# Optimization experiments

Hardware: AMD Instinct MI355X
Metric: run time of the kernel (lower is better)

## Reference

```python
import jax, jax.numpy as jnp
import numpy as np

D_K = 128


def setup_inputs() -> dict:
    key = jax.random.key(0)
    k = jax.random.split(key, 5)
    B, H, H_KV, S_Q, S_PAST, D = 2, 16, 4, 1024, 1024, D_K
    return {
        "Q": jax.random.normal(k[0], (B, H, S_Q, D), dtype=jnp.float32),
        "K": jax.random.normal(k[1], (B, H, S_Q, D), dtype=jnp.float32),
        "V": jax.random.normal(k[2], (B, H, S_Q, D), dtype=jnp.float32),
        "past_key": jax.random.normal(k[3], (B, H_KV, S_PAST, D), dtype=jnp.float32),
        "past_value": jax.random.normal(k[4], (B, H_KV, S_PAST, D), dtype=jnp.float32),
    }


def reference(Q, K, V, past_key, past_value):
    B, H, S_q, D = Q.shape
    H_kv = past_key.shape[1]
    n_groups = H // H_kv
    scale = 1.0 / jnp.sqrt(jnp.float32(D_K))

    # expand_grouped_kv: [B,H_kv,S,D] -> [B,H_kv,G,S,D] -> [B,H,S,D] == repeat along heads
    pk = jnp.repeat(past_key, n_groups, axis=1)
    pv = jnp.repeat(past_value, n_groups, axis=1)
    K_full = jnp.concatenate([pk, K], axis=2)   # [B,H,S_k,D]
    V_full = jnp.concatenate([pv, V], axis=2)
    present_key = K_full[:, ::n_groups]         # [B,H_kv,S_present,D]
    present_value = V_full[:, ::n_groups]

    S_k = K_full.shape[2]
    scores = jnp.einsum("bhqd,bhkd->bhqk", Q, K_full) * scale  # [B,H,S_q,S_k]
    start = S_k - S_q
    # torch.tril(ones(S_q,S_k), diagonal=start): key j visible iff j <= q + start
    causal = jnp.arange(S_k)[None, :] <= (jnp.arange(S_q)[:, None] + start)
    scores = jnp.where(causal[None, None], scores, jnp.float32(-jnp.inf))
    attn = jax.nn.softmax(scores, axis=-1)
    out = jnp.einsum("bhqk,bhkd->bhqd", attn, V_full)
    return out, present_key, present_value
```

## Files before the change

### kernel.cpp

```cpp
#include <hip/hip_runtime.h>
#include <hip/hip_bf16.h>

#define B_    2
#define H_    16
#define HKV_  4
#define SQ_   1024
#define SP_   1024
#define SK_   2048
#define D_    128
#define QBLK  64
#define KVBLK 64
#define TILEB 32768
#define NPAST 128
#define NTILES 640

typedef __attribute__((ext_vector_type(8))) __bf16 bf16x8;
typedef __attribute__((ext_vector_type(4))) __bf16 bf16x4;
typedef __attribute__((ext_vector_type(4))) float  f32x4;

__device__ inline __bf16 f2bf(float f) { return (__bf16)f; }

__device__ inline void gl_lds16(const char* g, char* l) {
    __builtin_amdgcn_global_load_lds(
        (const __attribute__((address_space(1))) void*)g,
        (__attribute__((address_space(3))) void*)l, 16, 0, 0);
}

__global__ __launch_bounds__(256)
void prep_kernel(const float* __restrict__ Kin, const float* __restrict__ Vin,
                 const float* __restrict__ PK,  const float* __restrict__ PV,
                 float* __restrict__ opk, float* __restrict__ opv, char* __restrict__ ws)
{
    __shared__ __align__(16) char Tl[TILEB];
    const int tid = threadIdx.x;
    const int id  = blockIdx.x;

    const float *ksrc, *vsrc;
    float *pkdst = nullptr, *pvdst = nullptr;
    size_t tidx;
    if (id < NPAST) {
        int grp = id & 7, kt = id >> 3;
        int s0 = kt * 64;
        ksrc = PK + (((size_t)grp)*SP_ + s0)*(size_t)D_;
        vsrc = PV + (((size_t)grp)*SP_ + s0)*(size_t)D_;
        pkdst = opk + (((size_t)grp)*SK_ + s0)*(size_t)D_;
        pvdst = opv + (((size_t)grp)*SK_ + s0)*(size_t)D_;
        tidx = (size_t)(grp*16 + kt);
    } else {
        int nid = id - NPAST;
        int h16 = nid >> 4;
        int ktp = nid & 15;
        int bb = h16 >> 4, hh = h16 & 15;
        int s0 = ktp * 64;
        ksrc = Kin + (((size_t)h16)*SQ_ + s0)*(size_t)D_;
        vsrc = Vin + (((size_t)h16)*SQ_ + s0)*(size_t)D_;
        if ((hh & 3) == 0) {
            int grp = bb*4 + (hh >> 2);
            pkdst = opk + (((size_t)grp)*SK_ + SP_ + s0)*(size_t)D_;
            pvdst = opv + (((size_t)grp)*SK_ + SP_ + s0)*(size_t)D_;
        }
        tidx = (size_t)(NPAST + nid);
    }

    #pragma unroll
    for (int i = 0; i < 4; ++i) {
        int idx = i*256 + tid, row = idx >> 4, c8 = idx & 15;
        f32x4 a0 = *(const f32x4*)(ksrc + row*D_ + c8*8);
        f32x4 a1 = *(const f32x4*)(ksrc + row*D_ + c8*8 + 4);
        if (pkdst) {
            *(f32x4*)(pkdst + row*D_ + c8*8)     = a0;
            *(f32x4*)(pkdst + row*D_ + c8*8 + 4) = a1;
        }
        bf16x8 f;
        #pragma unroll
        for (int j = 0; j < 4; ++j) { f[j] = f2bf(a0[j]); f[j+4] = f2bf(a1[j]); }
        int off = (row*256 + c8*16) ^ ((row & 7) << 4);
        *(bf16x8*)(Tl + off) = f;
    }
    #pragma unroll
    for (int i = 0; i < 2; ++i) {
        int blk = i*256 + tid, bk = blk & 15, bd = blk >> 4;
        f32x4 vr[4];
        #pragma unroll
        for (int kk = 0; kk < 4; ++kk)
            vr[kk] = *(const f32x4*)(vsrc + (4*bk+kk)*D_ + bd*4);
        #pragma unroll
        for (int j = 0; j < 4; ++j) {
            int d = 4*bd + j;
            bf16x4 t;
            t[0]=f2bf(vr[0][j]); t[1]=f2bf(vr[1][j]);
            t[2]=f2bf(vr[2][j]); t[3]=f2bf(vr[3][j]);
            int off = (d*128 + bk*8) ^ ((d & 7) << 4);
            *(bf16x4*)(Tl + 16384 + off) = t;
        }
    }
    if (pvdst) {
        #pragma unroll
        for (int i = 0; i < 4; ++i) {
            int idx = i*256 + tid, row = idx >> 4, c8 = idx & 15;
            *(f32x4*)(pvdst + row*D_ + c8*8)     = *(const f32x4*)(vsrc + row*D_ + c8*8);
            *(f32x4*)(pvdst + row*D_ + c8*8 + 4) = *(const f32x4*)(vsrc + row*D_ + c8*8 + 4);
        }
    }
    __syncthreads();
    char* dst = ws + tidx*TILEB;
    #pragma unroll
    for (int i = 0; i < 8; ++i) {
        int off = i*4096 + tid*16;
        *(f32x4*)(dst + off) = *(const f32x4*)(Tl + off);
    }
}

__global__ __launch_bounds__(256, 2)
void attn_lean_kernel(const float* __restrict__ Q, float* __restrict__ Out,
                      const char* __restrict__ ws)
{
    __shared__ __align__(16) char Kb2[2][16384];
    __shared__ __align__(16) char Vb2[2][16384];
    __shared__ __align__(16) char Pl[8192];

    const int tid = threadIdx.x;
    const int id  = blockIdx.x;
    const int grp  = id & 7;
    const int rest = id >> 3;
    const int hi   = rest & 3;
    const int qt   = rest >> 2;
    const int b    = grp >> 2;
    const int h    = (grp & 3)*4 + hi;
    const int h16  = b*16 + h;

    const int lane = tid & 63;
    const int w    = tid >> 6;
    const int lr   = lane & 15;
    const int lg   = lane >> 4;
    const int q0w  = qt * QBLK + w * 16;
    const int nt   = qt + 17;

    const float scale_l2e = 0.08838834764831845f * 1.4426950408889634f;

    const char* tiles = ws;
    const int boff = w*1024 + lane*16;
    auto STAGE = [&](int buf, int kt) {
        size_t t = (kt < 16) ? (size_t)(grp*16 + kt) : (size_t)(NPAST + h16*16 + (kt - 16));
        const char* src = tiles + t*TILEB;
        char* kb = Kb2[buf];
        char* vb = Vb2[buf];
        #pragma unroll
        for (int i = 0; i < 4; ++i) gl_lds16(src + i*4096 + boff,         kb + i*4096 + w*1024);
        #pragma unroll
        for (int i = 0; i < 4; ++i) gl_lds16(src + 16384 + i*4096 + boff, vb + i*4096 + w*1024);
    };

    STAGE(0, 0);

    bf16x8 qf[4];
    {
        const float* qsrc = Q + (((size_t)h16)*SQ_ + q0w + lr)*(size_t)D_ + lg*8;
        #pragma unroll
        for (int c = 0; c < 4; ++c) {
            f32x4 a0 = *(const f32x4*)(qsrc + c*32);
            f32x4 a1 = *(const f32x4*)(qsrc + c*32 + 4);
            bf16x8 f;
            #pragma unroll
            for (int j = 0; j < 4; ++j) {
                f[j]   = f2bf(a0[j] * scale_l2e);
                f[j+4] = f2bf(a1[j] * scale_l2e);
            }
            qf[c] = f;
        }
    }

    f32x4 o[8];
    #pragma unroll
    for (int i = 0; i < 8; ++i) o[i] = (f32x4){0.f,0.f,0.f,0.f};
    float m_r = -1e30f, l_r = 0.f;

    for (int kt = 0; kt < nt; ++kt) {
        const int cur = kt & 1;
        if (kt + 1 < nt) {
            STAGE(cur ^ 1, kt + 1);
            asm volatile("s_waitcnt vmcnt(8)" ::: "memory");
        } else {
            asm volatile("s_waitcnt vmcnt(0)" ::: "memory");
        }
        __builtin_amdgcn_sched_barrier(0);
        __builtin_amdgcn_s_barrier();
        __builtin_amdgcn_sched_barrier(0);

        const char* Kbp = Kb2[cur];
        const char* Vbp = Vb2[cur];

        f32x4 s[4];
        #pragma unroll
        for (int n = 0; n < 4; ++n) s[n] = (f32x4){0.f,0.f,0.f,0.f};
        #pragma unroll
        for (int n = 0; n < 4; ++n) {
            #pragma unroll
            for (int c = 0; c < 4; ++c) {
                int off = ((n*16 + lr)*256 + c*64 + lg*16) ^ ((lr & 7) << 4);
                bf16x8 kf = *(const bf16x8*)(Kbp + off);
                s[n] = __builtin_amdgcn_mfma_f32_16x16x32_bf16(kf, qf[c], s[n], 0, 0, 0);
            }
        }

        const int k0 = kt * KVBLK;
        float p[16];
        const bool needmask = (k0 + KVBLK - 1) > (q0w + SP_);
        if (needmask) {
            const int qv = q0w + lr + SP_;
            #pragma unroll
            for (int n = 0; n < 4; ++n)
                #pragma unroll
                for (int r = 0; r < 4; ++r) {
                    int kg = k0 + n*16 + lg*4 + r;
                    p[n*4+r] = (kg <= qv) ? s[n][r] : -1e30f;
                }
        } else {
            #pragma unroll
            for (int n = 0; n < 4; ++n)
                #pragma unroll
                for (int r = 0; r < 4; ++r) p[n*4+r] = s[n][r];
        }

        float mx = p[0];
        #pragma unroll
        for (int i = 1; i < 16; ++i) mx = fmaxf(mx, p[i]);
        mx = fmaxf(mx, __shfl_xor(mx, 16));
        mx = fmaxf(mx, __shfl_xor(mx, 32));
        if (!__all(mx <= m_r + 8.0f)) {
            float mnew  = fmaxf(m_r, mx);
            float alpha = exp2f(m_r - mnew);
            m_r = mnew;
            l_r *= alpha;
            #pragma unroll
            for (int dt = 0; dt < 8; ++dt) {
                o[dt][0] *= alpha; o[dt][1] *= alpha;
                o[dt][2] *= alpha; o[dt][3] *= alpha;
            }
        }
        float psum = 0.f;
        #pragma unroll
        for (int i = 0; i < 16; ++i) { p[i] = exp2f(p[i] - m_r); psum += p[i]; }
        psum += __shfl_xor(psum, 16);
        psum += __shfl_xor(psum, 32);
        l_r += psum;

        char* Pw = Pl + w*2048;
        #pragma unroll
        for (int n = 0; n < 4; ++n) {
            bf16x4 t;
            t[0]=f2bf(p[n*4+0]); t[1]=f2bf(p[n*4+1]);
            t[2]=f2bf(p[n*4+2]); t[3]=f2bf(p[n*4+3]);
            int off = (lr*128 + n*32 + lg*8) ^ ((lr & 7) << 4);
            *(bf16x4*)(Pw + off) = t;
        }

        #pragma unroll
        for (int kk = 0; kk < 2; ++kk) {
            int poff = (lr*128 + kk*64 + lg*16) ^ ((lr & 7) << 4);
            bf16x8 pa = *(const bf16x8*)(Pw + poff);
            #pragma unroll
            for (int dt = 0; dt < 8; ++dt) {
                int voff = ((dt*16 + lr)*128 + kk*64 + lg*16) ^ ((lr & 7) << 4);
                bf16x8 vf = *(const bf16x8*)(Vbp + voff);
                o[dt] = __builtin_amdgcn_mfma_f32_16x16x32_bf16(vf, pa, o[dt], 0, 0, 0);
            }
        }

        __builtin_amdgcn_sched_barrier(0);
        __builtin_amdgcn_s_barrier();
    }

    float inv = 1.0f / l_r;
    float* orow = Out + (((size_t)h16)*SQ_ + q0w + lr)*(size_t)D_;
    #pragma unroll
    for (int dt = 0; dt < 8; ++dt) {
        f32x4 st;
        st[0]=o[dt][0]*inv; st[1]=o[dt][1]*inv;
        st[2]=o[dt][2]*inv; st[3]=o[dt][3]*inv;
        *(f32x4*)(orow + dt*16 + lg*4) = st;
    }
}

__global__ __launch_bounds__(256, 2)
void attn_fallback_kernel(const float* __restrict__ Q, const float* __restrict__ Kin,
                          const float* __restrict__ Vin, const float* __restrict__ PK,
                          const float* __restrict__ PV, float* __restrict__ Out,
                          float* __restrict__ opk, float* __restrict__ opv)
{
    __shared__ __align__(16) __bf16 Klds[KVBLK * D_];
    __shared__ __align__(16) __bf16 Vlds[D_ * KVBLK];
    __shared__ __align__(16) __bf16 Plds[4 * 16 * KVBLK];

    const int tid = threadIdx.x;
    const int id  = blockIdx.x;

    if (id >= 512) {
        const int cid = id - 512;
        const int bgc = cid & 7;
        const int sub = cid >> 3;
        const int isV = sub >> 2;
        const int q4  = sub & 3;
        const int bb = bgc >> 2, g = bgc & 3;
        const float* past = isV ? PV : PK;
        const float* cur  = isV ? Vin : Kin;
        float* dst = isV ? opv : opk;
        const int base = bgc*65536 + q4*16384;
        #pragma unroll 4
        for (int i = 0; i < 64; ++i) {
            int id2 = base + i*256 + tid;
            int d4 = id2 & 31;
            int s  = (id2 >> 5) & (SK_-1);
            const float* srcp = (s < SP_)
                ? past + (((size_t)bgc)*SP_ + s)*(size_t)D_ + d4*4
                : cur  + (((size_t)(bb*H_ + 4*g))*SQ_ + (s - SP_))*(size_t)D_ + d4*4;
            float4 v = *(const float4*)srcp;
            *(float4*)(dst + (size_t)id2*4) = v;
        }
        return;
    }

    const int grp  = id & 7;
    const int rest = id >> 3;
    const int hi   = rest & 3;
    const int qt   = rest >> 2;
    const int b    = grp >> 2;
    const int h    = (grp & 3)*4 + hi;

    const int lane = tid & 63;
    const int w    = tid >> 6;
    const int lr   = lane & 15;
    const int lg   = lane >> 4;
    const int q0w  = qt * QBLK + w * 16;

    const float scale_l2e = 0.08838834764831845f * 1.4426950408889634f;

    bf16x8 qf[4];
    {
        const float* qsrc = Q + (((size_t)b*H_ + h)*SQ_ + q0w + lr)*(size_t)D_ + lg*8;
        #pragma unroll
        for (int c = 0; c < 4; ++c) {
            f32x4 a0 = *(const f32x4*)(qsrc + c*32);
            f32x4 a1 = *(const f32x4*)(qsrc + c*32 + 4);
            bf16x8 f;
            #pragma unroll
            for (int j = 0; j < 4; ++j) {
                f[j]   = f2bf(a0[j] * scale_l2e);
                f[j+4] = f2bf(a1[j] * scale_l2e);
            }
            qf[c] = f;
        }
    }

    f32x4 o[8];
    #pragma unroll
    for (int i = 0; i < 8; ++i) o[i] = (f32x4){0.f,0.f,0.f,0.f};
    float m_r = -1e30f, l_r = 0.f;

    const int nt = qt + 17;
    const size_t pk_base = (((size_t)b*HKV_ + (h>>2))*SP_)*(size_t)D_;
    const size_t kn_base = (((size_t)b*H_   + h     )*SQ_)*(size_t)D_;

    f32x4 kreg[4][2], vreg[2][4];
    auto loadKV = [&](const float* ks, const float* vs) {
        #pragma unroll
        for (int i = 0; i < 4; ++i) {
            int idx = i*256 + tid, row = idx >> 4, c8 = idx & 15;
            kreg[i][0] = *(const f32x4*)(ks + row*D_ + c8*8);
            kreg[i][1] = *(const f32x4*)(ks + row*D_ + c8*8 + 4);
        }
        #pragma unroll
        for (int i = 0; i < 2; ++i) {
            int blk = i*256 + tid, bk = blk & 15, bd = blk >> 4;
            #pragma unroll
            for (int kk = 0; kk < 4; ++kk)
                vreg[i][kk] = *(const f32x4*)(vs + (4*bk+kk)*D_ + bd*4);
        }
    };

    loadKV(PK + pk_base, PV + pk_base);

    for (int kt = 0; kt < nt; ++kt) {
        const int k0 = kt * KVBLK;
        __syncthreads();
        #pragma unroll
        for (int i = 0; i < 4; ++i) {
            int idx = i*256 + tid, row = idx >> 4, c8 = idx & 15;
            bf16x8 f;
            #pragma unroll
            for (int j = 0; j < 4; ++j) {
                f[j]   = f2bf(kreg[i][0][j]);
                f[j+4] = f2bf(kreg[i][1][j]);
            }
            int off = (row*256 + c8*16) ^ ((row & 7) << 4);
            *(bf16x8*)((char*)Klds + off) = f;
        }
        #pragma unroll
        for (int i = 0; i < 2; ++i) {
            int blk = i*256 + tid, bk = blk & 15, bd = blk >> 4;
            #pragma unroll
            for (int j = 0; j < 4; ++j) {
                int d = 4*bd + j;
                bf16x4 t;
                t[0]=f2bf(vreg[i][0][j]); t[1]=f2bf(vreg[i][1][j]);
                t[2]=f2bf(vreg[i][2][j]); t[3]=f2bf(vreg[i][3][j]);
                int off = (d*128 + bk*8) ^ ((d & 7) << 4);
                *(bf16x4*)((char*)Vlds + off) = t;
            }
        }
        __syncthreads();

        if (kt + 1 < nt) {
            const int k1 = k0 + KVBLK;
            const float* ks = (k1 < SP_) ? PK + pk_base + (size_t)k1*D_
                                         : Kin + kn_base + (size_t)(k1 - SP_)*D_;
            const float* vs = (k1 < SP_) ? PV + pk_base + (size_t)k1*D_
                                         : Vin + kn_base + (size_t)(k1 - SP_)*D_;
            loadKV(ks, vs);
        }

        f32x4 s[4];
        #pragma unroll
        for (int n = 0; n < 4; ++n) s[n] = (f32x4){0.f,0.f,0.f,0.f};
        #pragma unroll
        for (int n = 0; n < 4; ++n) {
            #pragma unroll
            for (int c = 0; c < 4; ++c) {
                int off = ((n*16 + lr)*256 + c*64 + lg*16) ^ ((lr & 7) << 4);
                bf16x8 kf = *(const bf16x8*)((char*)Klds + off);
                s[n] = __builtin_amdgcn_mfma_f32_16x16x32_bf16(kf, qf[c], s[n], 0, 0, 0);
            }
        }

        float p[16];
        const bool needmask = (k0 + KVBLK - 1) > (q0w + SP_);
        if (needmask) {
            const int qv = q0w + lr + SP_;
            #pragma unroll
            for (int n = 0; n < 4; ++n)
                #pragma unroll
                for (int r = 0; r < 4; ++r) {
                    int kg = k0 + n*16 + lg*4 + r;
                    p[n*4+r] = (kg <= qv) ? s[n][r] : -1e30f;
                }
        } else {
            #pragma unroll
            for (int n = 0; n < 4; ++n)
                #pragma unroll
                for (int r = 0; r < 4; ++r) p[n*4+r] = s[n][r];
        }

        float mx = p[0];
        #pragma unroll
        for (int i = 1; i < 16; ++i) mx = fmaxf(mx, p[i]);
        mx = fmaxf(mx, __shfl_xor(mx, 16));
        mx = fmaxf(mx, __shfl_xor(mx, 32));
        if (!__all(mx <= m_r + 8.0f)) {
            float mnew  = fmaxf(m_r, mx);
            float alpha = exp2f(m_r - mnew);
            m_r = mnew;
            l_r *= alpha;
            #pragma unroll
            for (int dt = 0; dt < 8; ++dt) {
                o[dt][0] *= alpha; o[dt][1] *= alpha;
                o[dt][2] *= alpha; o[dt][3] *= alpha;
            }
        }
        float psum = 0.f;
        #pragma unroll
        for (int i = 0; i < 16; ++i) { p[i] = exp2f(p[i] - m_r); psum += p[i]; }
        psum += __shfl_xor(psum, 16);
        psum += __shfl_xor(psum, 32);
        l_r += psum;

        char* Pw = (char*)Plds + w*2048;
        #pragma unroll
        for (int n = 0; n < 4; ++n) {
            bf16x4 t;
            t[0]=f2bf(p[n*4+0]); t[1]=f2bf(p[n*4+1]);
            t[2]=f2bf(p[n*4+2]); t[3]=f2bf(p[n*4+3]);
            int off = (lr*128 + n*32 + lg*8) ^ ((lr & 7) << 4);
            *(bf16x4*)(Pw + off) = t;
        }

        #pragma unroll
        for (int kk = 0; kk < 2; ++kk) {
            int poff = (lr*128 + kk*64 + lg*16) ^ ((lr & 7) << 4);
            bf16x8 pa = *(const bf16x8*)(Pw + poff);
            #pragma unroll
            for (int dt = 0; dt < 8; ++dt) {
                int voff = ((dt*16 + lr)*128 + kk*64 + lg*16) ^ ((lr & 7) << 4);
                bf16x8 vf = *(const bf16x8*)((char*)Vlds + voff);
                o[dt] = __builtin_amdgcn_mfma_f32_16x16x32_bf16(vf, pa, o[dt], 0, 0, 0);
            }
        }
    }

    float inv = 1.0f / l_r;
    float* orow = Out + (((size_t)b*H_ + h)*SQ_ + q0w + lr)*(size_t)D_;
    #pragma unroll
    for (int dt = 0; dt < 8; ++dt) {
        f32x4 st;
        st[0]=o[dt][0]*inv; st[1]=o[dt][1]*inv;
        st[2]=o[dt][2]*inv; st[3]=o[dt][3]*inv;
        *(f32x4*)(orow + dt*16 + lg*4) = st;
    }
}

extern "C" void kernel_launch(void* const* d_in, const int* in_sizes, int n_in,
                              void* d_out, int out_size, void* d_ws, size_t ws_size,
                              hipStream_t stream) {
    const float* Q   = (const float*)d_in[0];
    const float* K   = (const float*)d_in[1];
    const float* V   = (const float*)d_in[2];
    const float* PK  = (const float*)d_in[3];
    const float* PV  = (const float*)d_in[4];
    float* out = (float*)d_out;
    float* opk = out + (size_t)B_*H_*SQ_*D_;
    float* opv = opk + (size_t)B_*HKV_*SK_*D_;

    const size_t NEED = (size_t)NTILES * TILEB;
    if (ws_size >= NEED) {
        char* ws = (char*)d_ws;
        prep_kernel<<<NTILES, 256, 0, stream>>>(K, V, PK, PV, opk, opv, ws);
        attn_lean_kernel<<<512, 256, 0, stream>>>(Q, out, ws);
    } else {
        attn_fallback_kernel<<<576, 256, 0, stream>>>(Q, K, V, PK, PV, out, opk, opv);
    }
}
```

Before: 82.76 us.

## Split KV range into two halves per query tile with a combine kernel

Adds a split-KV attention path where each query tile's causal KV range is divided into two roughly equal halves, each handled by its own block (1024 blocks instead of 512). Partial outputs and running max/sum go to workspace, and a separate combine kernel merges them with rescaling. The goal is to balance the uneven causal workload and raise occupancy on the GPU. The cost is an extra kernel launch, extra global traffic for partial results, and single-buffered LDS staging. The path only runs when the workspace is large enough.

```diff
diff --git a/kernel.cpp b/kernel.cpp
--- a/kernel.cpp
+++ b/kernel.cpp
@@ -112,6 +112,227 @@
 }
 
 __global__ __launch_bounds__(256, 2)
+void attn_split_kernel(const float* __restrict__ Q, float* __restrict__ Out,
+                       const char* __restrict__ ws,
+                       float* __restrict__ wsO, float* __restrict__ wsML)
+{
+    __shared__ __align__(16) char Kb[16384];
+    __shared__ __align__(16) char Vb[16384];
+    __shared__ __align__(16) char Pl[8192];
+
+    const int tid = threadIdx.x;
+    const int id  = blockIdx.x;
+    const int grp   = id & 7;
+    const int rest  = id >> 3;
+    const int u     = rest & 31;
+    const int v     = rest >> 5;
+    const int qpair = u & 7;
+    const int hi    = u >> 3;
+    const int qt    = (v & 2) ? (15 - qpair) : qpair;
+    const int hf    = v & 1;
+    const int b     = grp >> 2;
+    const int h     = (grp & 3)*4 + hi;
+    const int h16   = b*16 + h;
+
+    const int lane = tid & 63;
+    const int w    = tid >> 6;
+    const int lr   = lane & 15;
+    const int lg   = lane >> 4;
+    const int q0w  = qt * QBLK + w * 16;
+
+    const int nt     = qt + 17;
+    const int ch     = (qt + 18) >> 1;
+    const int kt_beg = hf ? ch : 0;
+    const int kt_end = hf ? nt : ch;
+
+    const float scale_l2e = 0.08838834764831845f * 1.4426950408889634f;
+
+    const int boff = w*1024 + lane*16;
+    auto tile_src = [&](int kt) {
+        size_t t = (kt < 16) ? (size_t)(grp*16 + kt) : (size_t)(NPAST + h16*16 + (kt - 16));
+        return ws + t*TILEB;
+    };
+    auto STAGE_K = [&](int kt) {
+        const char* src = tile_src(kt);
+        #pragma unroll
+        for (int i = 0; i < 4; ++i) gl_lds16(src + i*4096 + boff, Kb + i*4096 + w*1024);
+    };
+    auto STAGE_V = [&](int kt) {
+        const char* src = tile_src(kt);
+        #pragma unroll
+        for (int i = 0; i < 4; ++i) gl_lds16(src + 16384 + i*4096 + boff, Vb + i*4096 + w*1024);
+    };
+
+    const float* qsrc = Q + (((size_t)h16)*SQ_ + q0w + lr)*(size_t)D_ + lg*8;
+    f32x4 qa[4][2];
+    #pragma unroll
+    for (int c = 0; c < 4; ++c) {
+        qa[c][0] = *(const f32x4*)(qsrc + c*32);
+        qa[c][1] = *(const f32x4*)(qsrc + c*32 + 4);
+    }
+    STAGE_K(kt_beg);
+    STAGE_V(kt_beg);
+
+    bf16x8 qf[4];
+    #pragma unroll
+    for (int c = 0; c < 4; ++c) {
+        bf16x8 f;
+        #pragma unroll
+        for (int j = 0; j < 4; ++j) {
+            f[j]   = f2bf(qa[c][0][j] * scale_l2e);
+            f[j+4] = f2bf(qa[c][1][j] * scale_l2e);
+        }
+        qf[c] = f;
+    }
+
+    f32x4 o[8];
+    #pragma unroll
+    for (int i = 0; i < 8; ++i) o[i] = (f32x4){0.f,0.f,0.f,0.f};
+    float m_r = -1e30f, l_r = 0.f;
+
+    for (int kt = kt_beg; kt < kt_end; ++kt) {
+        asm volatile("s_waitcnt vmcnt(4)" ::: "memory");
+        __builtin_amdgcn_sched_barrier(0);
+        __builtin_amdgcn_s_barrier();
+        __builtin_amdgcn_sched_barrier(0);
+
+        f32x4 s[4];
+        #pragma unroll
+        for (int n = 0; n < 4; ++n) s[n] = (f32x4){0.f,0.f,0.f,0.f};
+        #pragma unroll
+        for (int n = 0; n < 4; ++n) {
+            #pragma unroll
+            for (int c = 0; c < 4; ++c) {
+                int off = ((n*16 + lr)*256 + c*64 + lg*16) ^ ((lr & 7) << 4);
+                bf16x8 kf = *(const bf16x8*)(Kb + off);
+                s[n] = __builtin_amdgcn_mfma_f32_16x16x32_bf16(kf, qf[c], s[n], 0, 0, 0);
+            }
+        }
+
+        asm volatile("s_waitcnt vmcnt(0)" ::: "memory");
+        __builtin_amdgcn_sched_barrier(0);
+        __builtin_amdgcn_s_barrier();
+        __builtin_amdgcn_sched_barrier(0);
+        if (kt + 1 < kt_end) STAGE_K(kt + 1);
+
+        const int k0 = kt * KVBLK;
+        float p[16];
+        const bool needmask = (k0 + KVBLK - 1) > (q0w + SP_);
+        if (needmask) {
+            const int qv = q0w + lr + SP_;
+            #pragma unroll
+            for (int n = 0; n < 4; ++n)
+                #pragma unroll
+                for (int r = 0; r < 4; ++r) {
+                    int kg = k0 + n*16 + lg*4 + r;
+                    p[n*4+r] = (kg <= qv) ? s[n][r] : -1e30f;
+                }
+        } else {
+            #pragma unroll
+            for (int n = 0; n < 4; ++n)
+                #pragma unroll
+                for (int r = 0; r < 4; ++r) p[n*4+r] = s[n][r];
+        }
+
+        float mx = p[0];
+        #pragma unroll
+        for (int i = 1; i < 16; ++i) mx = fmaxf(mx, p[i]);
+        mx = fmaxf(mx, __shfl_xor(mx, 16));
+        mx = fmaxf(mx, __shfl_xor(mx, 32));
+        if (!__all(mx <= m_r + 8.0f)) {
+            float mnew  = fmaxf(m_r, mx);
+            float alpha = exp2f(m_r - mnew);
+            m_r = mnew;
+            l_r *= alpha;
+            #pragma unroll
+            for (int dt = 0; dt < 8; ++dt) {
+                o[dt][0] *= alpha; o[dt][1] *= alpha;
+                o[dt][2] *= alpha; o[dt][3] *= alpha;
+            }
+        }
+        float psum = 0.f;
+        #pragma unroll
+        for (int i = 0; i < 16; ++i) { p[i] = exp2f(p[i] - m_r); psum += p[i]; }
+        psum += __shfl_xor(psum, 16);
+        psum += __shfl_xor(psum, 32);
+        l_r += psum;
+
+        char* Pw = Pl + w*2048;
+        #pragma unroll
+        for (int n = 0; n < 4; ++n) {
+            bf16x4 t;
+            t[0]=f2bf(p[n*4+0]); t[1]=f2bf(p[n*4+1]);
+            t[2]=f2bf(p[n*4+2]); t[3]=f2bf(p[n*4+3]);
+            int off = (lr*128 + n*32 + lg*8) ^ ((lr & 7) << 4);
+            *(bf16x4*)(Pw + off) = t;
+        }
+
+        #pragma unroll
+        for (int kk = 0; kk < 2; ++kk) {
+            int poff = (lr*128 + kk*64 + lg*16) ^ ((lr & 7) << 4);
+            bf16x8 pa = *(const bf16x8*)(Pw + poff);
+            #pragma unroll
+            for (int dt = 0; dt < 8; ++dt) {
+                int voff = ((dt*16 + lr)*128 + kk*64 + lg*16) ^ ((lr & 7) << 4);
+                bf16x8 vf = *(const bf16x8*)(Vb + voff);
+                o[dt] = __builtin_amdgcn_mfma_f32_16x16x32_bf16(vf, pa, o[dt], 0, 0, 0);
+            }
+        }
+
+        __builtin_amdgcn_sched_barrier(0);
+        __builtin_amdgcn_s_barrier();
+        __builtin_amdgcn_sched_barrier(0);
+        if (kt + 1 < kt_end) STAGE_V(kt + 1);
+    }
+
+    const int slot = (h16*16 + qt)*2 + hf;
+    float* Oh = wsO + (size_t)slot*8192 + (size_t)(w*16 + lr)*128;
+    #pragma unroll
+    for (int dt = 0; dt < 8; ++dt)
+        *(f32x4*)(Oh + dt*16 + lg*4) = o[dt];
+    if (lg == 0) {
+        wsML[(size_t)slot*128 + (w*16 + lr)*2]     = m_r;
+        wsML[(size_t)slot*128 + (w*16 + lr)*2 + 1] = l_r;
+    }
+}
+
+__global__ __launch_bounds__(256)
+void combine_kernel(const float* __restrict__ wsO, const float* __restrict__ wsML,
+                    float* __restrict__ Out)
+{
+    const int p   = blockIdx.x;
+    const int tid = threadIdx.x;
+    __shared__ float sml[64][2];
+    if (tid < 64) {
+        int s0 = (p*2    )*128 + tid*2;
+        int s1 = (p*2 + 1)*128 + tid*2;
+        float m1 = wsML[s0], l1 = wsML[s0+1];
+        float m2 = wsML[s1], l2 = wsML[s1+1];
+        float m  = fmaxf(m1, m2);
+        float a1 = exp2f(m1 - m), a2 = exp2f(m2 - m);
+        float inv = 1.0f / (l1*a1 + l2*a2);
+        sml[tid][0] = a1 * inv;
+        sml[tid][1] = a2 * inv;
+    }
+    __syncthreads();
+    const float* O1 = wsO + (size_t)(p*2    )*8192;
+    const float* O2 = wsO + (size_t)(p*2 + 1)*8192;
+    float* dst = Out + (size_t)p*8192;
+    #pragma unroll
+    for (int i = 0; i < 8; ++i) {
+        int v = i*256 + tid;
+        int row = v >> 5;
+        f32x4 x1 = *(const f32x4*)(O1 + (size_t)v*4);
+        f32x4 x2 = *(const f32x4*)(O2 + (size_t)v*4);
+        float a1 = sml[row][0], a2 = sml[row][1];
+        f32x4 r;
+        r[0]=x1[0]*a1+x2[0]*a2; r[1]=x1[1]*a1+x2[1]*a2;
+        r[2]=x1[2]*a1+x2[2]*a2; r[3]=x1[3]*a1+x2[3]*a2;
+        *(f32x4*)(dst + (size_t)v*4) = r;
+    }
+}
+
+__global__ __launch_bounds__(256, 2)
 void attn_lean_kernel(const float* __restrict__ Q, float* __restrict__ Out,
                       const char* __restrict__ ws)
 {
@@ -138,17 +359,14 @@
 
     const float scale_l2e = 0.08838834764831845f * 1.4426950408889634f;
 
-    const char* tiles = ws;
     const int boff = w*1024 + lane*16;
     auto STAGE = [&](int buf, int kt) {
         size_t t = (kt < 16) ? (size_t)(grp*16 + kt) : (size_t)(NPAST + h16*16 + (kt - 16));
-        const char* src = tiles + t*TILEB;
-        char* kb = Kb2[buf];
-        char* vb = Vb2[buf];
-        #pragma unroll
-        for (int i = 0; i < 4; ++i) gl_lds16(src + i*4096 + boff,         kb + i*4096 + w*1024);
-        #pragma unroll
-        for (int i = 0; i < 4; ++i) gl_lds16(src + 16384 + i*4096 + boff, vb + i*4096 + w*1024);
+        const char* src = ws + t*TILEB;
+        #pragma unroll
+        for (int i = 0; i < 4; ++i) gl_lds16(src + i*4096 + boff,         Kb2[buf] + i*4096 + w*1024);
+        #pragma unroll
+        for (int i = 0; i < 4; ++i) gl_lds16(src + 16384 + i*4096 + boff, Vb2[buf] + i*4096 + w*1024);
     };
 
     STAGE(0, 0);
@@ -519,8 +737,16 @@
     float* opk = out + (size_t)B_*H_*SQ_*D_;
     float* opv = opk + (size_t)B_*HKV_*SK_*D_;
 
-    const size_t NEED = (size_t)NTILES * TILEB;
-    if (ws_size >= NEED) {
+    const size_t TILES_B = (size_t)NTILES * TILEB;
+    const size_t SPLIT_B = TILES_B + (size_t)1024*8192*4 + (size_t)1024*128*4;
+    if (ws_size >= SPLIT_B) {
+        char*  ws   = (char*)d_ws;
+        float* wsO  = (float*)(ws + TILES_B);
+        float* wsML = wsO + (size_t)1024*8192;
+        prep_kernel<<<NTILES, 256, 0, stream>>>(K, V, PK, PV, opk, opv, ws);
+        attn_split_kernel<<<1024, 256, 0, stream>>>(Q, out, ws, wsO, wsML);
+        combine_kernel<<<512, 256, 0, stream>>>(wsO, wsML, out);
+    } else if (ws_size >= TILES_B) {
         char* ws = (char*)d_ws;
         prep_kernel<<<NTILES, 256, 0, stream>>>(K, V, PK, PV, opk, opv, ws);
         attn_lean_kernel<<<512, 256, 0, stream>>>(Q, out, ws);
```

Result: slower. 94.36 us (+14.0%).

## Switch to 32x32 MFMA tiles with split-KV halves and combine pass

Applied to the files above, without the earlier changes.

The attention kernel now uses 32x32x16 bf16 MFMA with 128-query blocks per workgroup. Each block's KV range is split into two halves handled by separate workgroups, and a combine kernel merges them using per-row m/l values. The goal is to balance causal work across workgroups and to raise MFMA efficiency through larger tiles. The K/V tile swizzle layout changes to match. The cost is an extra kernel launch plus writing and reading partial outputs in fp32 workspace.

```diff
diff --git a/kernel.cpp b/kernel.cpp
--- a/kernel.cpp
+++ b/kernel.cpp
@@ -8,15 +8,15 @@
 #define SP_   1024
 #define SK_   2048
 #define D_    128
-#define QBLK  64
 #define KVBLK 64
 #define TILEB 32768
 #define NPAST 128
 #define NTILES 640
 
-typedef __attribute__((ext_vector_type(8))) __bf16 bf16x8;
-typedef __attribute__((ext_vector_type(4))) __bf16 bf16x4;
-typedef __attribute__((ext_vector_type(4))) float  f32x4;
+typedef __attribute__((ext_vector_type(8)))  __bf16 bf16x8;
+typedef __attribute__((ext_vector_type(4)))  __bf16 bf16x4;
+typedef __attribute__((ext_vector_type(4)))  float  f32x4;
+typedef __attribute__((ext_vector_type(16))) float  f32x16;
 
 __device__ inline __bf16 f2bf(float f) { return (__bf16)f; }
 
@@ -74,7 +74,7 @@
         bf16x8 f;
         #pragma unroll
         for (int j = 0; j < 4; ++j) { f[j] = f2bf(a0[j]); f[j+4] = f2bf(a1[j]); }
-        int off = (row*256 + c8*16) ^ ((row & 7) << 4);
+        int off = row*256 + ((c8*16) ^ ((row & 15) << 4));
         *(bf16x8*)(Tl + off) = f;
     }
     #pragma unroll
@@ -87,10 +87,11 @@
         #pragma unroll
         for (int j = 0; j < 4; ++j) {
             int d = 4*bd + j;
+            int r = d & 63, half = d >> 6;
             bf16x4 t;
             t[0]=f2bf(vr[0][j]); t[1]=f2bf(vr[1][j]);
             t[2]=f2bf(vr[2][j]); t[3]=f2bf(vr[3][j]);
-            int off = (d*128 + bk*8) ^ ((d & 7) << 4);
+            int off = r*256 + ((half*128 + 8*bk) ^ ((r & 15) << 4));
             *(bf16x4*)(Tl + 16384 + off) = t;
         }
     }
@@ -112,37 +113,42 @@
 }
 
 __global__ __launch_bounds__(256, 2)
-void attn_lean_kernel(const float* __restrict__ Q, float* __restrict__ Out,
-                      const char* __restrict__ ws)
+void attn32_kernel(const float* __restrict__ Q, const char* __restrict__ ws,
+                   float* __restrict__ wsO, float* __restrict__ wsML)
 {
     __shared__ __align__(16) char Kb2[2][16384];
     __shared__ __align__(16) char Vb2[2][16384];
-    __shared__ __align__(16) char Pl[8192];
+    __shared__ __align__(16) char Pl[16384];
 
     const int tid = threadIdx.x;
     const int id  = blockIdx.x;
     const int grp  = id & 7;
     const int rest = id >> 3;
-    const int hi   = rest & 3;
-    const int qt   = rest >> 2;
+    const int hi4  = rest & 3;
+    const int qt   = 7 - ((rest >> 2) & 7);
+    const int hf   = rest >> 5;
     const int b    = grp >> 2;
-    const int h    = (grp & 3)*4 + hi;
+    const int h    = (grp & 3)*4 + hi4;
     const int h16  = b*16 + h;
 
     const int lane = tid & 63;
     const int w    = tid >> 6;
-    const int lr   = lane & 15;
-    const int lg   = lane >> 4;
-    const int q0w  = qt * QBLK + w * 16;
-    const int nt   = qt + 17;
+    const int l31  = lane & 31;
+    const int hi   = lane >> 5;
+    const int swzm = (l31 & 15) << 4;
+    const int q0w  = qt*128 + w*32;
+
+    const int nt     = 2*qt + 18;
+    const int ch     = qt + 9;
+    const int kt_beg = hf ? ch : 0;
+    const int kt_end = hf ? nt : ch;
 
     const float scale_l2e = 0.08838834764831845f * 1.4426950408889634f;
 
-    const char* tiles = ws;
     const int boff = w*1024 + lane*16;
     auto STAGE = [&](int buf, int kt) {
         size_t t = (kt < 16) ? (size_t)(grp*16 + kt) : (size_t)(NPAST + h16*16 + (kt - 16));
-        const char* src = tiles + t*TILEB;
+        const char* src = ws + t*TILEB;
         char* kb = Kb2[buf];
         char* vb = Vb2[buf];
         #pragma unroll
@@ -151,15 +157,15 @@
         for (int i = 0; i < 4; ++i) gl_lds16(src + 16384 + i*4096 + boff, vb + i*4096 + w*1024);
     };
 
-    STAGE(0, 0);
-
-    bf16x8 qf[4];
+    STAGE(0, kt_beg);
+
+    bf16x8 qf[8];
     {
-        const float* qsrc = Q + (((size_t)h16)*SQ_ + q0w + lr)*(size_t)D_ + lg*8;
-        #pragma unroll
-        for (int c = 0; c < 4; ++c) {
-            f32x4 a0 = *(const f32x4*)(qsrc + c*32);
-            f32x4 a1 = *(const f32x4*)(qsrc + c*32 + 4);
+        const float* qsrc = Q + ((size_t)h16*SQ_ + q0w + l31)*(size_t)D_;
+        #pragma unroll
+        for (int c = 0; c < 8; ++c) {
+            f32x4 a0 = *(const f32x4*)(qsrc + c*16 + hi*8);
+            f32x4 a1 = *(const f32x4*)(qsrc + c*16 + hi*8 + 4);
             bf16x8 f;
             #pragma unroll
             for (int j = 0; j < 4; ++j) {
@@ -170,14 +176,18 @@
         }
     }
 
-    f32x4 o[8];
-    #pragma unroll
-    for (int i = 0; i < 8; ++i) o[i] = (f32x4){0.f,0.f,0.f,0.f};
+    f32x16 o2[4];
+    #pragma unroll
+    for (int i = 0; i < 4; ++i)
+        #pragma unroll
+        for (int j = 0; j < 16; ++j) o2[i][j] = 0.f;
     float m_r = -1e30f, l_r = 0.f;
 
-    for (int kt = 0; kt < nt; ++kt) {
-        const int cur = kt & 1;
-        if (kt + 1 < nt) {
+    char* Pw = Pl + w*4096;
+
+    for (int kt = kt_beg; kt < kt_end; ++kt) {
+        const int cur = (kt - kt_beg) & 1;
+        if (kt + 1 < kt_end) {
             STAGE(cur ^ 1, kt + 1);
             asm volatile("s_waitcnt vmcnt(8)" ::: "memory");
         } else {
@@ -190,42 +200,37 @@
         const char* Kbp = Kb2[cur];
         const char* Vbp = Vb2[cur];
 
-        f32x4 s[4];
-        #pragma unroll
-        for (int n = 0; n < 4; ++n) s[n] = (f32x4){0.f,0.f,0.f,0.f};
-        #pragma unroll
-        for (int n = 0; n < 4; ++n) {
-            #pragma unroll
-            for (int c = 0; c < 4; ++c) {
-                int off = ((n*16 + lr)*256 + c*64 + lg*16) ^ ((lr & 7) << 4);
-                bf16x8 kf = *(const bf16x8*)(Kbp + off);
-                s[n] = __builtin_amdgcn_mfma_f32_16x16x32_bf16(kf, qf[c], s[n], 0, 0, 0);
-            }
+        f32x16 s[2];
+        #pragma unroll
+        for (int c2 = 0; c2 < 2; ++c2)
+            #pragma unroll
+            for (int j = 0; j < 16; ++j) s[c2][j] = 0.f;
+        #pragma unroll
+        for (int c = 0; c < 8; ++c) {
+            int cb = (c*32 + hi*16) ^ swzm;
+            bf16x8 kf0 = *(const bf16x8*)(Kbp + l31*256 + cb);
+            s[0] = __builtin_amdgcn_mfma_f32_32x32x16_bf16(kf0, qf[c], s[0], 0, 0, 0);
+            bf16x8 kf1 = *(const bf16x8*)(Kbp + 8192 + l31*256 + cb);
+            s[1] = __builtin_amdgcn_mfma_f32_32x32x16_bf16(kf1, qf[c], s[1], 0, 0, 0);
         }
 
         const int k0 = kt * KVBLK;
-        float p[16];
-        const bool needmask = (k0 + KVBLK - 1) > (q0w + SP_);
-        if (needmask) {
-            const int qv = q0w + lr + SP_;
-            #pragma unroll
-            for (int n = 0; n < 4; ++n)
+        if ((k0 + KVBLK - 1) > (q0w + SP_)) {
+            const int qv = q0w + l31 + SP_;
+            #pragma unroll
+            for (int c2 = 0; c2 < 2; ++c2)
                 #pragma unroll
-                for (int r = 0; r < 4; ++r) {
-                    int kg = k0 + n*16 + lg*4 + r;
-                    p[n*4+r] = (kg <= qv) ? s[n][r] : -1e30f;
+                for (int r = 0; r < 16; ++r) {
+                    int kg = k0 + 32*c2 + (r & 3) + 8*(r >> 2) + 4*hi;
+                    if (kg > qv) s[c2][r] = -1e30f;
                 }
-        } else {
-            #pragma unroll
-            for (int n = 0; n < 4; ++n)
-                #pragma unroll
-                for (int r = 0; r < 4; ++r) p[n*4+r] = s[n][r];
-        }
-
-        float mx = p[0];
-        #pragma unroll
-        for (int i = 1; i < 16; ++i) mx = fmaxf(mx, p[i]);
-        mx = fmaxf(mx, __shfl_xor(mx, 16));
+        }
+
+        float mx = s[0][0];
+        #pragma unroll
+        for (int c2 = 0; c2 < 2; ++c2)
+            #pragma unroll
+            for (int r = 0; r < 16; ++r) mx = fmaxf(mx, s[c2][r]);
         mx = fmaxf(mx, __shfl_xor(mx, 32));
         if (!__all(mx <= m_r + 8.0f)) {
             float mnew  = fmaxf(m_r, mx);
@@ -233,37 +238,43 @@
             m_r = mnew;
             l_r *= alpha;
             #pragma unroll
-            for (int dt = 0; dt < 8; ++dt) {
-                o[dt][0] *= alpha; o[dt][1] *= alpha;
-                o[dt][2] *= alpha; o[dt][3] *= alpha;
-            }
+            for (int i = 0; i < 4; ++i)
+                #pragma unroll
+                for (int j = 0; j < 16; ++j) o2[i][j] *= alpha;
         }
         float psum = 0.f;
         #pragma unroll
-        for (int i = 0; i < 16; ++i) { p[i] = exp2f(p[i] - m_r); psum += p[i]; }
-        psum += __shfl_xor(psum, 16);
+        for (int c2 = 0; c2 < 2; ++c2)
+            #pragma unroll
+            for (int r = 0; r < 16; ++r) {
+                float e = exp2f(s[c2][r] - m_r);
+                s[c2][r] = e;
+                psum += e;
+            }
         psum += __shfl_xor(psum, 32);
         l_r += psum;
 
-        char* Pw = Pl + w*2048;
-        #pragma unroll
-        for (int n = 0; n < 4; ++n) {
-            bf16x4 t;
-            t[0]=f2bf(p[n*4+0]); t[1]=f2bf(p[n*4+1]);
-            t[2]=f2bf(p[n*4+2]); t[3]=f2bf(p[n*4+3]);
-            int off = (lr*128 + n*32 + lg*8) ^ ((lr & 7) << 4);
-            *(bf16x4*)(Pw + off) = t;
-        }
-
-        #pragma unroll
-        for (int kk = 0; kk < 2; ++kk) {
-            int poff = (lr*128 + kk*64 + lg*16) ^ ((lr & 7) << 4);
-            bf16x8 pa = *(const bf16x8*)(Pw + poff);
-            #pragma unroll
-            for (int dt = 0; dt < 8; ++dt) {
-                int voff = ((dt*16 + lr)*128 + kk*64 + lg*16) ^ ((lr & 7) << 4);
-                bf16x8 vf = *(const bf16x8*)(Vbp + voff);
-                o[dt] = __builtin_amdgcn_mfma_f32_16x16x32_bf16(vf, pa, o[dt], 0, 0, 0);
+        #pragma unroll
+        for (int c2 = 0; c2 < 2; ++c2)
+            #pragma unroll
+            for (int rq = 0; rq < 4; ++rq) {
+                bf16x4 t;
+                t[0]=f2bf(s[c2][rq*4+0]); t[1]=f2bf(s[c2][rq*4+1]);
+                t[2]=f2bf(s[c2][rq*4+2]); t[3]=f2bf(s[c2][rq*4+3]);
+                int off = l31*128 + ((c2*64 + rq*16 + hi*8) ^ ((l31 & 7) << 4));
+                *(bf16x4*)(Pw + off) = t;
+            }
+
+        #pragma unroll
+        for (int ks = 0; ks < 4; ++ks) {
+            int poff = l31*128 + ((ks*32 + hi*16) ^ ((l31 & 7) << 4));
+            bf16x8 pf = *(const bf16x8*)(Pw + poff);
+            #pragma unroll
+            for (int dblk = 0; dblk < 4; ++dblk) {
+                int r = (dblk & 1)*32 + l31;
+                int off = r*256 + ((((dblk >> 1)*128) + ks*32 + hi*16) ^ swzm);
+                bf16x8 vf = *(const bf16x8*)(Vbp + off);
+                o2[dblk] = __builtin_amdgcn_mfma_f32_32x32x16_bf16(vf, pf, o2[dblk], 0, 0, 0);
             }
         }
 
@@ -271,14 +282,57 @@
         __builtin_amdgcn_s_barrier();
     }
 
-    float inv = 1.0f / l_r;
-    float* orow = Out + (((size_t)h16)*SQ_ + q0w + lr)*(size_t)D_;
-    #pragma unroll
-    for (int dt = 0; dt < 8; ++dt) {
-        f32x4 st;
-        st[0]=o[dt][0]*inv; st[1]=o[dt][1]*inv;
-        st[2]=o[dt][2]*inv; st[3]=o[dt][3]*inv;
-        *(f32x4*)(orow + dt*16 + lg*4) = st;
+    const int slot = (h16*8 + qt)*2 + hf;
+    const int q    = w*32 + l31;
+    float* Oh = wsO + (size_t)slot*16384 + (size_t)q*128;
+    #pragma unroll
+    for (int dblk = 0; dblk < 4; ++dblk)
+        #pragma unroll
+        for (int rg = 0; rg < 4; ++rg) {
+            f32x4 st;
+            st[0] = o2[dblk][rg*4+0]; st[1] = o2[dblk][rg*4+1];
+            st[2] = o2[dblk][rg*4+2]; st[3] = o2[dblk][rg*4+3];
+            *(f32x4*)(Oh + dblk*32 + rg*8 + hi*4) = st;
+        }
+    if (hi == 0) {
+        wsML[(size_t)slot*256 + q*2]     = m_r;
+        wsML[(size_t)slot*256 + q*2 + 1] = l_r;
+    }
+}
+
+__global__ __launch_bounds__(256)
+void combine_kernel(const float* __restrict__ wsO, const float* __restrict__ wsML,
+                    float* __restrict__ Out)
+{
+    const int p   = blockIdx.x;
+    const int tid = threadIdx.x;
+    __shared__ float sml[128][2];
+    if (tid < 128) {
+        size_t s0 = (size_t)(p*2    )*256 + tid*2;
+        size_t s1 = (size_t)(p*2 + 1)*256 + tid*2;
+        float m1 = wsML[s0], l1 = wsML[s0+1];
+        float m2 = wsML[s1], l2 = wsML[s1+1];
+        float m  = fmaxf(m1, m2);
+        float a1 = exp2f(m1 - m), a2 = exp2f(m2 - m);
+        float inv = 1.0f / (l1*a1 + l2*a2);
+        sml[tid][0] = a1 * inv;
+        sml[tid][1] = a2 * inv;
+    }
+    __syncthreads();
+    const float* O1 = wsO + (size_t)(p*2    )*16384;
+    const float* O2 = wsO + (size_t)(p*2 + 1)*16384;
+    float* dst = Out + (size_t)p*16384;
+    #pragma unroll
+    for (int i = 0; i < 16; ++i) {
+        int v = i*256 + tid;
+        int row = v >> 5;
+        f32x4 x1 = *(const f32x4*)(O1 + (size_t)v*4);
+        f32x4 x2 = *(const f32x4*)(O2 + (size_t)v*4);
+        float a1 = sml[row][0], a2 = sml[row][1];
+        f32x4 r;
+        r[0]=x1[0]*a1+x2[0]*a2; r[1]=x1[1]*a1+x2[1]*a2;
+        r[2]=x1[2]*a1+x2[2]*a2; r[3]=x1[3]*a1+x2[3]*a2;
+        *(f32x4*)(dst + (size_t)v*4) = r;
     }
 }
 
@@ -331,7 +385,7 @@
     const int w    = tid >> 6;
     const int lr   = lane & 15;
     const int lg   = lane >> 4;
-    const int q0w  = qt * QBLK + w * 16;
+    const int q0w  = qt * 64 + w * 16;
 
     const float scale_l2e = 0.08838834764831845f * 1.4426950408889634f;
 
@@ -519,11 +573,15 @@
     float* opk = out + (size_t)B_*H_*SQ_*D_;
     float* opv = opk + (size_t)B_*HKV_*SK_*D_;
 
-    const size_t NEED = (size_t)NTILES * TILEB;
+    const size_t TILES_B = (size_t)NTILES * TILEB;
+    const size_t NEED = TILES_B + (size_t)512*16384*4 + (size_t)512*256*4;
     if (ws_size >= NEED) {
-        char* ws = (char*)d_ws;
+        char*  ws   = (char*)d_ws;
+        float* wsO  = (float*)(ws + TILES_B);
+        float* wsML = wsO + (size_t)512*16384;
         prep_kernel<<<NTILES, 256, 0, stream>>>(K, V, PK, PV, opk, opv, ws);
-        attn_lean_kernel<<<512, 256, 0, stream>>>(Q, out, ws);
+        attn32_kernel<<<512, 256, 0, stream>>>(Q, ws, wsO, wsML);
+        combine_kernel<<<256, 256, 0, stream>>>(wsO, wsML, out);
     } else {
         attn_fallback_kernel<<<576, 256, 0, stream>>>(Q, K, V, PK, PV, out, opk, opv);
     }
```

Measured after the change: 82.76 us. About the same (-0.0%).
